# Performance work log

Hardware: AMD Instinct MI355X
Metric: run time of the kernel (lower is better)

## Reference

```python
import jax, jax.numpy as jnp
import numpy as np

N = 50000
E = 800000
D_IN = 1000
D_H2 = 128  # h_dim * multiple
D_H = 16


def gat_conv(x, src, dst, W, attn_l, attn_r, bias, n):
    """DGL-style GATConv (no dropout, no activation). Returns [n, H, F]."""
    H, F = attn_l.shape
    feat = (x @ W).reshape(n, H, F)                      # [N,H,F]
    el = jnp.sum(feat * attn_l[None], axis=-1)           # [N,H]
    er = jnp.sum(feat * attn_r[None], axis=-1)           # [N,H]
    e = jax.nn.leaky_relu(el[src] + er[dst], 0.2)        # [E,H]
    emax = jax.ops.segment_max(e, dst, num_segments=n)   # [N,H] per-dst softmax max
    ee = jnp.exp(e - emax[dst])                          # [E,H]
    denom = jax.ops.segment_sum(ee, dst, num_segments=n) # [N,H]
    alpha = ee / denom[dst]                              # [E,H]
    msg = feat[src] * alpha[..., None]                   # [E,H,F]
    out = jax.ops.segment_sum(msg, dst, num_segments=n)  # [N,H,F]
    return out + bias.reshape(1, H, F)


def setup_inputs() -> dict:
    key = jax.random.key(0)
    ks = jax.random.split(key, 24)
    rn = lambda k, shp, s=0.05: (jax.random.normal(k, shp, dtype=jnp.float32) * s)
    inp = {
        "x": rn(ks[0], (N, D_IN), 1.0),
        "src": jax.random.randint(ks[1], (E,), 0, N, dtype=jnp.int32),
        "dst": jax.random.randint(ks[2], (E,), 0, N, dtype=jnp.int32),
        "W1": rn(ks[3], (D_IN, D_H2)),
        "al1": rn(ks[4], (1, D_H2)),
        "ar1": rn(ks[5], (1, D_H2)),
        "b1": jnp.zeros((D_H2,), jnp.float32),
        "W2": rn(ks[6], (D_H2, 2 * D_H2)),
        "al2": rn(ks[7], (2, D_H2)),
        "ar2": rn(ks[8], (2, D_H2)),
        "b2": jnp.zeros((2 * D_H2,), jnp.float32),
        "Wm": rn(ks[9], (D_H2, 2 * D_H)),
        "alm": rn(ks[10], (2, D_H)),
        "arm": rn(ks[11], (2, D_H)),
        "bm": jnp.zeros((2 * D_H,), jnp.float32),
        "Wv": rn(ks[12], (D_H2, 2 * D_H)),
        "alv": rn(ks[13], (2, D_H)),
        "arv": rn(ks[14], (2, D_H)),
        "bv": jnp.zeros((2 * D_H,), jnp.float32),
        "eps": rn(ks[15], (N, D_H), 1.0),
    }
    return inp


def reference(x, src, dst, W1, al1, ar1, b1, W2, al2, ar2, b2,
              Wm, alm, arm, bm, Wv, alv, arv, bv, eps):
    n = x.shape[0]
    o = gat_conv(x, src, dst, W1, al1, ar1, b1, n).mean(-2)           # [N,128]
    o = gat_conv(o, src, dst, W2, al2, ar2, b2, n).mean(-2) + o       # residual
    mean = gat_conv(o, src, dst, Wm, alm, arm, bm, n).mean(-2)        # [N,16]
    var = jnp.exp(gat_conv(o, src, dst, Wv, alv, arv, bv, n).mean(-2))
    z = mean + jnp.sqrt(var) * eps                                    # reparameterize
    return z, mean, var
```

## Files before the change

### kernel.cpp

```cpp
#include <hip/hip_runtime.h>
#include <hip/hip_bf16.h>
#include <math.h>

typedef unsigned short u16;
typedef unsigned int u32;
typedef __attribute__((ext_vector_type(8))) __bf16 bf16x8;
typedef __attribute__((ext_vector_type(4))) float f32x4;
typedef __attribute__((ext_vector_type(4))) u32 u32x4;

#define NNODES 50000
#define NEDGES 800000

__device__ __forceinline__ float bf2f(u16 u) {
    union { u32 i; float f; } v; v.i = ((u32)u) << 16; return v.f;
}
__device__ __forceinline__ u16 f2bf(float x) {
    union { float f; u32 i; } v; v.f = x;
    u32 r = v.i + 0x7fffu + ((v.i >> 16) & 1u);
    return (u16)(r >> 16);
}
__device__ __forceinline__ float lrelu(float x) { return x >= 0.f ? x : 0.2f * x; }

__global__ __launch_bounds__(256) void k_zero(int* a, int count) {
    int i = blockIdx.x * 256 + threadIdx.x;
    if (i < count) a[i] = 0;
}

__global__ __launch_bounds__(256) void k_count(const int* __restrict__ dst, int* __restrict__ counts, int e) {
    int i = blockIdx.x * 256 + threadIdx.x;
    if (i < e) atomicAdd(&counts[dst[i]], 1);
}

__global__ __launch_bounds__(256) void k_scan1(const int* __restrict__ counts, int* __restrict__ row_ptr,
                                               int* __restrict__ bsums, int n) {
    __shared__ int tmp[256];
    int t = threadIdx.x, i = blockIdx.x * 256 + t;
    int v = (i < n) ? counts[i] : 0;
    tmp[t] = v; __syncthreads();
    for (int off = 1; off < 256; off <<= 1) {
        int x = 0; if (t >= off) x = tmp[t - off];
        __syncthreads(); tmp[t] += x; __syncthreads();
    }
    if (i < n) row_ptr[i] = tmp[t] - v;
    if (t == 255) bsums[blockIdx.x] = tmp[255];
}

__global__ __launch_bounds__(256) void k_scan2(int* bsums, int nb) {
    __shared__ int tmp[256];
    int t = threadIdx.x;
    int v = (t < nb) ? bsums[t] : 0;
    tmp[t] = v; __syncthreads();
    for (int off = 1; off < 256; off <<= 1) {
        int x = 0; if (t >= off) x = tmp[t - off];
        __syncthreads(); tmp[t] += x; __syncthreads();
    }
    if (t < nb) bsums[t] = tmp[t] - v;
}

__global__ __launch_bounds__(256) void k_scan3(int* __restrict__ row_ptr, const int* __restrict__ bsums,
                                               int n, int total) {
    int i = blockIdx.x * 256 + threadIdx.x;
    if (i < n) row_ptr[i] += bsums[blockIdx.x];
    if (i == 0) row_ptr[n] = total;
}

__global__ __launch_bounds__(256) void k_fill(const int* __restrict__ src, const int* __restrict__ dst,
                                              const int* __restrict__ row_ptr, int* __restrict__ cursor,
                                              int* __restrict__ esrc, int e) {
    int i = blockIdx.x * 256 + threadIdx.x;
    if (i < e) {
        int d = dst[i];
        int p = row_ptr[d] + atomicAdd(&cursor[d], 1);
        esrc[p] = src[i];
    }
}

__global__ __launch_bounds__(256) void k_transpose(const float* __restrict__ W, u16* __restrict__ Wt, int K, int Nn) {
    int i = blockIdx.x * 256 + threadIdx.x;
    if (i < K * Nn) { int k = i / Nn, n = i % Nn; Wt[n * K + k] = f2bf(W[i]); }
}

__global__ __launch_bounds__(256) void k_attnvec(const float* __restrict__ W2, const float* __restrict__ al2,
                                                 const float* __restrict__ ar2, const float* __restrict__ b2,
                                                 float* __restrict__ ul, float* __restrict__ ur,
                                                 float* __restrict__ bmean) {
    int t = threadIdx.x;
    int h = t >> 7, k = t & 127;
    const float* wrow = W2 + (size_t)k * 256 + h * 128;
    const float* alh = al2 + h * 128;
    const float* arh = ar2 + h * 128;
    float sl = 0.f, sr = 0.f;
    for (int f = 0; f < 128; f += 4) {
        f32x4 w = *(const f32x4*)(wrow + f);
        f32x4 a = *(const f32x4*)(alh + f);
        f32x4 r = *(const f32x4*)(arh + f);
#pragma unroll
        for (int q = 0; q < 4; q++) { sl += w[q] * a[q]; sr += w[q] * r[q]; }
    }
    ul[t] = sl; ur[t] = sr;
    if (t < 128) bmean[t] = 0.5f * (b2[t] + b2[128 + t]);
}

__global__ __launch_bounds__(256) void k_makeWc(const float* __restrict__ W2, u16* __restrict__ Wct) {
    int i = blockIdx.x * 256 + threadIdx.x;
    if (i < 128 * 256) {
        int f = i >> 8, c = i & 255, h = c >> 7, k = c & 127;
        Wct[i] = f2bf(0.5f * W2[(size_t)k * 256 + h * 128 + f]);
    }
}

__device__ __forceinline__ void load_af(const float* __restrict__ arow, int k0, int K, bf16x8& a) {
    if (k0 + 8 <= K) {
        f32x4 a0 = *(const f32x4*)(arow + k0);
        f32x4 a1 = *(const f32x4*)(arow + k0 + 4);
#pragma unroll
        for (int j = 0; j < 4; j++) { a[j] = (__bf16)a0[j]; a[4 + j] = (__bf16)a1[j]; }
    } else {
#pragma unroll
        for (int j = 0; j < 8; j++) a[j] = (__bf16)0.f;
    }
}
__device__ __forceinline__ void load_af(const u16* __restrict__ arow, int k0, int K, bf16x8& a) {
    if (k0 + 8 <= K) a = *(const bf16x8*)(arow + k0);
    else {
#pragma unroll
        for (int j = 0; j < 8; j++) a[j] = (__bf16)0.f;
    }
}

template <typename AT, bool EPI>
__global__ __launch_bounds__(256) void k_gemm_tiled(const AT* __restrict__ A, const u16* __restrict__ Bt,
                                                    u16* __restrict__ C, int M, int Nn, int K,
                                                    const float* __restrict__ bias,
                                                    const u16* __restrict__ resid) {
    __shared__ __align__(16) u16 lb[2][128 * 40];
    const int tid = threadIdx.x;
    const int wave = tid >> 6, lane = tid & 63;
    const int m = lane & 15, quad = lane >> 4;
    const int row0 = blockIdx.x * 64 + wave * 16;
    const int col0 = blockIdx.y * 128;

    f32x4 acc[8];
#pragma unroll
    for (int t = 0; t < 8; t++)
#pragma unroll
        for (int r = 0; r < 4; r++) acc[t][r] = 0.f;

    int ar = row0 + m; if (ar > M - 1) ar = M - 1;
    const AT* arow = A + (size_t)ar * K;
    const int scol = tid & 127;
    const int sseg = (tid >> 7) * 16;
    const u16* bcol = Bt + (size_t)(col0 + scol) * K;

    const int nsteps = (K + 31) >> 5;

#pragma unroll
    for (int p = 0; p < 2; ++p) {
        int kl = sseg + p * 8;
        u32x4 v = 0;
        if (kl < K) v = *(const u32x4*)(bcol + kl);
        *(u32x4*)&lb[0][scol * 40 + kl] = v;
    }
    bf16x8 acur, anext;
    load_af(arow, quad * 8, K, acur);
    __syncthreads();

    for (int s = 0; s < nsteps; ++s) {
        const int buf = s & 1;
        if (s + 1 < nsteps) {
            const int k0n = (s + 1) * 32;
            load_af(arow, k0n + quad * 8, K, anext);
#pragma unroll
            for (int p = 0; p < 2; ++p) {
                int kl = sseg + p * 8;
                u32x4 v = 0;
                if (k0n + kl < K) v = *(const u32x4*)(bcol + k0n + kl);
                *(u32x4*)&lb[buf ^ 1][scol * 40 + kl] = v;
            }
        }
#pragma unroll
        for (int t = 0; t < 8; ++t) {
            bf16x8 b = *(const bf16x8*)&lb[buf][(t * 16 + m) * 40 + quad * 8];
            acc[t] = __builtin_amdgcn_mfma_f32_16x16x32_bf16(acur, b, acc[t], 0, 0, 0);
        }
        acur = anext;
        __syncthreads();
    }

#pragma unroll
    for (int t = 0; t < 8; t++)
#pragma unroll
        for (int r = 0; r < 4; r++) {
            int row = row0 + quad * 4 + r;
            int col = col0 + t * 16 + m;
            if (row < M) {
                float v = acc[t][r];
                if (EPI) v += bias[col] + bf2f(resid[(size_t)row * Nn + col]);
                C[(size_t)row * Nn + col] = f2bf(v);
            }
        }
}

template <int NT>
__global__ __launch_bounds__(64) void k_gemm(const u16* __restrict__ A, const u16* __restrict__ Bt,
                                             u16* __restrict__ C, int M, int Nn, int K) {
    int row0 = blockIdx.x * 16;
    int col0 = blockIdx.y * (16 * NT);
    int lane = threadIdx.x;
    int m = lane & 15, quad = lane >> 4;
    f32x4 acc[NT];
#pragma unroll
    for (int t = 0; t < NT; t++)
#pragma unroll
        for (int r = 0; r < 4; r++) acc[t][r] = 0.f;

    const u16* arow = A + (size_t)(row0 + m) * K + quad * 8;
    int full = K >> 5;
    for (int s = 0; s < full; ++s) {
        bf16x8 a = *(const bf16x8*)(arow + s * 32);
#pragma unroll
        for (int t = 0; t < NT; t++) {
            bf16x8 b = *(const bf16x8*)(Bt + (size_t)(col0 + t * 16 + m) * K + s * 32 + quad * 8);
            acc[t] = __builtin_amdgcn_mfma_f32_16x16x32_bf16(a, b, acc[t], 0, 0, 0);
        }
    }
#pragma unroll
    for (int t = 0; t < NT; t++)
#pragma unroll
        for (int r = 0; r < 4; r++) {
            int row = row0 + quad * 4 + r;
            int col = col0 + t * 16 + m;
            if (row < M) C[(size_t)row * Nn + col] = f2bf(acc[t][r]);
        }
}

__global__ __launch_bounds__(256) void k_eler1(const u16* __restrict__ feat, const float* __restrict__ al,
                                               const float* __restrict__ ar, float* __restrict__ el,
                                               float* __restrict__ er, int n) {
    int node = blockIdx.x * 4 + (threadIdx.x >> 6);
    if (node >= n) return;
    int lane = threadIdx.x & 63;
    const u16* fr = feat + (size_t)node * 128;
    float f0 = bf2f(fr[lane]), f1 = bf2f(fr[64 + lane]);
    float pe = f0 * al[lane] + f1 * al[64 + lane];
    float pr = f0 * ar[lane] + f1 * ar[64 + lane];
#pragma unroll
    for (int off = 32; off; off >>= 1) { pe += __shfl_xor(pe, off); pr += __shfl_xor(pr, off); }
    if (lane == 0) { el[node] = pe; er[node] = pr; }
}

__global__ __launch_bounds__(256) void k_eler2o(const u16* __restrict__ o_in, const float* __restrict__ ul,
                                                const float* __restrict__ ur, float* __restrict__ el,
                                                float* __restrict__ er, int n) {
    int node = blockIdx.x * 4 + (threadIdx.x >> 6);
    if (node >= n) return;
    int lane = threadIdx.x & 63;
    const u16* fr = o_in + (size_t)node * 128;
    float f0 = bf2f(fr[lane]), f1 = bf2f(fr[64 + lane]);
#pragma unroll
    for (int h = 0; h < 2; ++h) {
        float pe = f0 * ul[h * 128 + lane] + f1 * ul[h * 128 + 64 + lane];
        float pr = f0 * ur[h * 128 + lane] + f1 * ur[h * 128 + 64 + lane];
#pragma unroll
        for (int off = 32; off; off >>= 1) { pe += __shfl_xor(pe, off); pr += __shfl_xor(pr, off); }
        if (lane == 0) { el[node * 2 + h] = pe; er[node * 2 + h] = pr; }
    }
}

__global__ __launch_bounds__(256) void k_elermv(const u16* __restrict__ featm, const u16* __restrict__ featv,
                                                const float* __restrict__ alm, const float* __restrict__ arm,
                                                const float* __restrict__ alv, const float* __restrict__ arv,
                                                float* __restrict__ elm, float* __restrict__ erm,
                                                float* __restrict__ elv, float* __restrict__ erv, int n) {
    int node = blockIdx.x * 4 + (threadIdx.x >> 6);
    if (node >= n) return;
    int lane = threadIdx.x & 63;
    int tbl = lane >> 5, j = lane & 31;
    const u16* ft = tbl ? featv : featm;
    const float* al = tbl ? alv : alm;
    const float* ar = tbl ? arv : arm;
    float f = bf2f(ft[(size_t)node * 32 + j]);
    float pe = f * al[j], pr = f * ar[j];
#pragma unroll
    for (int off = 1; off < 16; off <<= 1) { pe += __shfl_xor(pe, off); pr += __shfl_xor(pr, off); }
    if ((lane & 15) == 0) {
        int h = (lane >> 4) & 1;
        float* el = tbl ? elv : elm; float* er = tbl ? erv : erm;
        el[node * 2 + h] = pe; er[node * 2 + h] = pr;
    }
}

__global__ __launch_bounds__(256) void k_agg1(const int* __restrict__ row_ptr, const int* __restrict__ esrc,
                                              const u16* __restrict__ feat, const float* __restrict__ el,
                                              const float* __restrict__ er, const float* __restrict__ bias,
                                              u16* __restrict__ o_bf, int n) {
    int node = blockIdx.x * 4 + (threadIdx.x >> 6);
    if (node >= n) return;
    int lane = threadIdx.x & 63;
    int beg = row_ptr[node], end = row_ptr[node + 1];
    float erd = er[node];
    float mx = -3.0e38f;
    for (int i = beg + lane; i < end; i += 64) mx = fmaxf(mx, el[esrc[i]]);
#pragma unroll
    for (int off = 32; off; off >>= 1) mx = fmaxf(mx, __shfl_xor(mx, off));
    float me = (end > beg) ? lrelu(mx + erd) : 0.f;
    float acc0 = 0.f, acc1 = 0.f, den = 0.f;
    for (int base = beg; base < end; base += 64) {
        int i = base + lane;
        float w = 0.f; int s = 0;
        if (i < end) { s = esrc[i]; w = expf(lrelu(el[s] + erd) - me); }
        den += w;
        int cnt = min(64, end - base);
        int j = 0;
        for (; j + 4 <= cnt; j += 4) {
            float w0 = __shfl(w, j), w1 = __shfl(w, j + 1), w2 = __shfl(w, j + 2), w3 = __shfl(w, j + 3);
            int s0 = __shfl(s, j), s1 = __shfl(s, j + 1), s2 = __shfl(s, j + 2), s3 = __shfl(s, j + 3);
            u32 p0 = ((const u32*)(feat + (size_t)s0 * 128))[lane];
            u32 p1 = ((const u32*)(feat + (size_t)s1 * 128))[lane];
            u32 p2 = ((const u32*)(feat + (size_t)s2 * 128))[lane];
            u32 p3 = ((const u32*)(feat + (size_t)s3 * 128))[lane];
            acc0 += w0 * bf2f((u16)(p0 & 0xffff)) + w1 * bf2f((u16)(p1 & 0xffff))
                  + w2 * bf2f((u16)(p2 & 0xffff)) + w3 * bf2f((u16)(p3 & 0xffff));
            acc1 += w0 * bf2f((u16)(p0 >> 16)) + w1 * bf2f((u16)(p1 >> 16))
                  + w2 * bf2f((u16)(p2 >> 16)) + w3 * bf2f((u16)(p3 >> 16));
        }
        for (; j < cnt; ++j) {
            float wj = __shfl(w, j);
            int sj = __shfl(s, j);
            u32 pv = ((const u32*)(feat + (size_t)sj * 128))[lane];
            acc0 += wj * bf2f((u16)(pv & 0xffff));
            acc1 += wj * bf2f((u16)(pv >> 16));
        }
    }
#pragma unroll
    for (int off = 32; off; off >>= 1) den += __shfl_xor(den, off);
    float inv = (den > 0.f) ? 1.f / den : 0.f;
    float o0 = acc0 * inv + bias[2 * lane];
    float o1 = acc1 * inv + bias[2 * lane + 1];
    u32 pv = (u32)f2bf(o0) | ((u32)f2bf(o1) << 16);
    ((u32*)(o_bf + (size_t)node * 128))[lane] = pv;
}

__global__ __launch_bounds__(256) void k_agg2o(const int* __restrict__ row_ptr, const int* __restrict__ esrc,
                                               const u16* __restrict__ o_in, const float* __restrict__ el,
                                               const float* __restrict__ er, u16* __restrict__ agg, int n) {
    int node = blockIdx.x * 4 + (threadIdx.x >> 6);
    if (node >= n) return;
    int lane = threadIdx.x & 63;
    int beg = row_ptr[node], end = row_ptr[node + 1];
    float er0 = er[node * 2], er1 = er[node * 2 + 1];
    float mx0 = -3.0e38f, mx1 = -3.0e38f;
    for (int i = beg + lane; i < end; i += 64) {
        int s = esrc[i];
        float2 e2 = *(const float2*)(el + 2 * s);
        mx0 = fmaxf(mx0, e2.x); mx1 = fmaxf(mx1, e2.y);
    }
#pragma unroll
    for (int off = 32; off; off >>= 1) { mx0 = fmaxf(mx0, __shfl_xor(mx0, off)); mx1 = fmaxf(mx1, __shfl_xor(mx1, off)); }
    float me0 = (end > beg) ? lrelu(mx0 + er0) : 0.f;
    float me1 = (end > beg) ? lrelu(mx1 + er1) : 0.f;
    float a00 = 0.f, a01 = 0.f, a10 = 0.f, a11 = 0.f, d0 = 0.f, d1 = 0.f;
    for (int base = beg; base < end; base += 64) {
        int i = base + lane;
        float w0 = 0.f, w1 = 0.f; int s = 0;
        if (i < end) {
            s = esrc[i];
            float2 e2 = *(const float2*)(el + 2 * s);
            w0 = expf(lrelu(e2.x + er0) - me0);
            w1 = expf(lrelu(e2.y + er1) - me1);
        }
        d0 += w0; d1 += w1;
        int cnt = min(64, end - base);
        int j = 0;
        for (; j + 4 <= cnt; j += 4) {
            float w0a = __shfl(w0, j), w0b = __shfl(w0, j + 1), w0c = __shfl(w0, j + 2), w0d = __shfl(w0, j + 3);
            float w1a = __shfl(w1, j), w1b = __shfl(w1, j + 1), w1c = __shfl(w1, j + 2), w1d = __shfl(w1, j + 3);
            int sa = __shfl(s, j), sb = __shfl(s, j + 1), sc = __shfl(s, j + 2), sd = __shfl(s, j + 3);
            u32 pa = ((const u32*)(o_in + (size_t)sa * 128))[lane];
            u32 pb = ((const u32*)(o_in + (size_t)sb * 128))[lane];
            u32 pc = ((const u32*)(o_in + (size_t)sc * 128))[lane];
            u32 pd = ((const u32*)(o_in + (size_t)sd * 128))[lane];
            float la = bf2f((u16)(pa & 0xffff)), ha = bf2f((u16)(pa >> 16));
            float lb = bf2f((u16)(pb & 0xffff)), hb = bf2f((u16)(pb >> 16));
            float lc = bf2f((u16)(pc & 0xffff)), hc = bf2f((u16)(pc >> 16));
            float ld = bf2f((u16)(pd & 0xffff)), hd = bf2f((u16)(pd >> 16));
            a00 += w0a * la + w0b * lb + w0c * lc + w0d * ld;
            a01 += w0a * ha + w0b * hb + w0c * hc + w0d * hd;
            a10 += w1a * la + w1b * lb + w1c * lc + w1d * ld;
            a11 += w1a * ha + w1b * hb + w1c * hc + w1d * hd;
        }
        for (; j < cnt; ++j) {
            float w0j = __shfl(w0, j), w1j = __shfl(w1, j);
            int sj = __shfl(s, j);
            u32 pv = ((const u32*)(o_in + (size_t)sj * 128))[lane];
            float lo = bf2f((u16)(pv & 0xffff)), hi = bf2f((u16)(pv >> 16));
            a00 += w0j * lo; a01 += w0j * hi;
            a10 += w1j * lo; a11 += w1j * hi;
        }
    }
#pragma unroll
    for (int off = 32; off; off >>= 1) { d0 += __shfl_xor(d0, off); d1 += __shfl_xor(d1, off); }
    float i0 = (d0 > 0.f) ? 1.f / d0 : 0.f, i1 = (d1 > 0.f) ? 1.f / d1 : 0.f;
    u32 p0 = (u32)f2bf(a00 * i0) | ((u32)f2bf(a01 * i0) << 16);
    u32 p1 = (u32)f2bf(a10 * i1) | ((u32)f2bf(a11 * i1) << 16);
    u32* aw = (u32*)(agg + (size_t)node * 256);
    aw[lane] = p0;
    aw[64 + lane] = p1;
}

__global__ __launch_bounds__(256) void k_aggmv(const int* __restrict__ row_ptr, const int* __restrict__ esrc,
                                               const u16* __restrict__ featm, const u16* __restrict__ featv,
                                               const float* __restrict__ elm, const float* __restrict__ erm,
                                               const float* __restrict__ elv, const float* __restrict__ erv,
                                               const float* __restrict__ bm, const float* __restrict__ bv,
                                               const float* __restrict__ eps, float* __restrict__ out, int n) {
    int node = blockIdx.x * 4 + (threadIdx.x >> 6);
    if (node >= n) return;
    int lane = threadIdx.x & 63;
    int f = lane & 15, h = (lane >> 4) & 1, tbl = lane >> 5;
    int beg = row_ptr[node], end = row_ptr[node + 1];
    float erm0 = erm[2 * node], erm1 = erm[2 * node + 1];
    float erv0 = erv[2 * node], erv1 = erv[2 * node + 1];
    float mm0 = -3.0e38f, mm1 = -3.0e38f, mv0 = -3.0e38f, mv1 = -3.0e38f;
    for (int i = beg + lane; i < end; i += 64) {
        int s = esrc[i];
        float2 em = *(const float2*)(elm + 2 * s);
        float2 ev = *(const float2*)(elv + 2 * s);
        mm0 = fmaxf(mm0, em.x); mm1 = fmaxf(mm1, em.y);
        mv0 = fmaxf(mv0, ev.x); mv1 = fmaxf(mv1, ev.y);
    }
#pragma unroll
    for (int off = 32; off; off >>= 1) {
        mm0 = fmaxf(mm0, __shfl_xor(mm0, off)); mm1 = fmaxf(mm1, __shfl_xor(mm1, off));
        mv0 = fmaxf(mv0, __shfl_xor(mv0, off)); mv1 = fmaxf(mv1, __shfl_xor(mv1, off));
    }
    float mem0 = (end > beg) ? lrelu(mm0 + erm0) : 0.f;
    float mem1 = (end > beg) ? lrelu(mm1 + erm1) : 0.f;
    float mev0 = (end > beg) ? lrelu(mv0 + erv0) : 0.f;
    float mev1 = (end > beg) ? lrelu(mv1 + erv1) : 0.f;

    const u16* ftp = tbl ? featv : featm;
    const int fidx = h * 16 + f;
    float accv = 0.f;
    float dm0 = 0.f, dm1 = 0.f, dv0 = 0.f, dv1 = 0.f;
    for (int base = beg; base < end; base += 64) {
        int i = base + lane;
        float wm0 = 0.f, wm1 = 0.f, wv0 = 0.f, wv1 = 0.f; int s = 0;
        if (i < end) {
            s = esrc[i];
            float2 em = *(const float2*)(elm + 2 * s);
            float2 ev = *(const float2*)(elv + 2 * s);
            wm0 = expf(lrelu(em.x + erm0) - mem0);
            wm1 = expf(lrelu(em.y + erm1) - mem1);
            wv0 = expf(lrelu(ev.x + erv0) - mev0);
            wv1 = expf(lrelu(ev.y + erv1) - mev1);
        }
        dm0 += wm0; dm1 += wm1; dv0 += wv0; dv1 += wv1;
        int cnt = min(64, end - base);
        for (int j = 0; j < cnt; ++j) {
            int sj = __shfl(s, j);
            float bm0 = __shfl(wm0, j);
            float bm1 = __shfl(wm1, j);
            float bv0 = __shfl(wv0, j);
            float bv1 = __shfl(wv1, j);
            float wj = tbl ? (h ? bv1 : bv0) : (h ? bm1 : bm0);
            accv += wj * bf2f(ftp[(size_t)sj * 32 + fidx]);
        }
    }
#pragma unroll
    for (int off = 32; off; off >>= 1) {
        dm0 += __shfl_xor(dm0, off); dm1 += __shfl_xor(dm1, off);
        dv0 += __shfl_xor(dv0, off); dv1 += __shfl_xor(dv1, off);
    }
    float den = tbl ? (h ? dv1 : dv0) : (h ? dm1 : dm0);
    float inv = (den > 0.f) ? 1.f / den : 0.f;
    float biasc = tbl ? bv[fidx] : bm[fidx];
    float outc = accv * inv + biasc;
    float hm = 0.5f * (outc + __shfl_xor(outc, 16));
    float meanv = __shfl(hm, f);
    float varp = __shfl(hm, 32 + f);
    if (lane < 16) {
        float var = expf(varp);
        float z = meanv + sqrtf(var) * eps[(size_t)node * 16 + f];
        size_t base = (size_t)node * 16 + f;
        out[base] = z;
        out[(size_t)NNODES * 16 + base] = meanv;
        out[(size_t)2 * NNODES * 16 + base] = var;
    }
}

extern "C" void kernel_launch(void* const* d_in, const int* in_sizes, int n_in,
                              void* d_out, int out_size, void* d_ws, size_t ws_size,
                              hipStream_t stream) {
    const int N = NNODES, E = NEDGES;
    const float* x   = (const float*)d_in[0];
    const int* src   = (const int*)d_in[1];
    const int* dst   = (const int*)d_in[2];
    const float* W1  = (const float*)d_in[3];
    const float* al1 = (const float*)d_in[4];
    const float* ar1 = (const float*)d_in[5];
    const float* b1  = (const float*)d_in[6];
    const float* W2  = (const float*)d_in[7];
    const float* al2 = (const float*)d_in[8];
    const float* ar2 = (const float*)d_in[9];
    const float* b2  = (const float*)d_in[10];
    const float* Wm  = (const float*)d_in[11];
    const float* alm = (const float*)d_in[12];
    const float* arm = (const float*)d_in[13];
    const float* bm  = (const float*)d_in[14];
    const float* Wv  = (const float*)d_in[15];
    const float* alv = (const float*)d_in[16];
    const float* arv = (const float*)d_in[17];
    const float* bv  = (const float*)d_in[18];
    const float* eps = (const float*)d_in[19];
    float* out = (float*)d_out;

    char* ws = (char*)d_ws;
    size_t off = 0;
    auto take = [&](size_t bytes) { size_t r = off; off += (bytes + 255) & ~(size_t)255; return r; };
    int* counts   = (int*)(ws + take((size_t)N * 4));
    int* cursor   = (int*)(ws + take((size_t)N * 4));
    int* row_ptr  = (int*)(ws + take((size_t)(N + 1) * 4));
    int* bsums    = (int*)(ws + take(256 * 4));
    int* esrc     = (int*)(ws + take((size_t)E * 4));
    u16* W1t      = (u16*)(ws + take((size_t)128 * 1000 * 2));
    u16* Wct      = (u16*)(ws + take((size_t)128 * 256 * 2));
    u16* Wmt      = (u16*)(ws + take((size_t)32 * 128 * 2));
    u16* Wvt      = (u16*)(ws + take((size_t)32 * 128 * 2));
    float* ul2    = (float*)(ws + take(256 * 4));
    float* ur2    = (float*)(ws + take(256 * 4));
    float* bmean  = (float*)(ws + take(128 * 4));
    float* el1    = (float*)(ws + take((size_t)N * 4));
    float* er1    = (float*)(ws + take((size_t)N * 4));
    float* el2    = (float*)(ws + take((size_t)N * 2 * 4));
    float* er2    = (float*)(ws + take((size_t)N * 2 * 4));
    float* elm    = (float*)(ws + take((size_t)N * 2 * 4));
    float* erm    = (float*)(ws + take((size_t)N * 2 * 4));
    float* elv    = (float*)(ws + take((size_t)N * 2 * 4));
    float* erv    = (float*)(ws + take((size_t)N * 2 * 4));
    u16* o_bf     = (u16*)(ws + take((size_t)N * 128 * 2));
    u16* o2_bf    = (u16*)(ws + take((size_t)N * 128 * 2));
    u16* R        = (u16*)(ws + take((size_t)N * 256 * 2));
    u16* feat1    = R;
    u16* agg      = R;
    u16* featm    = R;
    u16* featv    = R + (size_t)N * 32;
    (void)ws_size; (void)n_in; (void)in_sizes; (void)out_size;

    const int nb = (N + 255) / 256;
    const int eb = (E + 255) / 256;
    const int wb = (N + 3) / 4;
    const int gb = (N + 63) / 64;

    k_zero<<<dim3(nb), 256, 0, stream>>>(counts, N);
    k_zero<<<dim3(nb), 256, 0, stream>>>(cursor, N);
    k_count<<<dim3(eb), 256, 0, stream>>>(dst, counts, E);
    k_scan1<<<dim3(nb), 256, 0, stream>>>(counts, row_ptr, bsums, N);
    k_scan2<<<dim3(1), 256, 0, stream>>>(bsums, nb);
    k_scan3<<<dim3(nb), 256, 0, stream>>>(row_ptr, bsums, N, E);
    k_fill<<<dim3(eb), 256, 0, stream>>>(src, dst, row_ptr, cursor, esrc, E);

    k_transpose<<<dim3((1000 * 128 + 255) / 256), 256, 0, stream>>>(W1, W1t, 1000, 128);
    k_makeWc<<<dim3(128), 256, 0, stream>>>(W2, Wct);
    k_attnvec<<<dim3(1), 256, 0, stream>>>(W2, al2, ar2, b2, ul2, ur2, bmean);
    k_transpose<<<dim3((128 * 32 + 255) / 256), 256, 0, stream>>>(Wm, Wmt, 128, 32);
    k_transpose<<<dim3((128 * 32 + 255) / 256), 256, 0, stream>>>(Wv, Wvt, 128, 32);

    k_gemm_tiled<float, false><<<dim3(gb, 1), 256, 0, stream>>>(x, W1t, feat1, N, 128, 1000, nullptr, nullptr);
    k_eler1<<<dim3(wb), 256, 0, stream>>>(feat1, al1, ar1, el1, er1, N);
    k_agg1<<<dim3(wb), 256, 0, stream>>>(row_ptr, esrc, feat1, el1, er1, b1, o_bf, N);

    k_eler2o<<<dim3(wb), 256, 0, stream>>>(o_bf, ul2, ur2, el2, er2, N);
    k_agg2o<<<dim3(wb), 256, 0, stream>>>(row_ptr, esrc, o_bf, el2, er2, agg, N);
    k_gemm_tiled<u16, true><<<dim3(gb, 1), 256, 0, stream>>>(agg, Wct, o2_bf, N, 128, 256, bmean, o_bf);

    k_gemm<2><<<dim3(N / 16, 1), 64, 0, stream>>>(o2_bf, Wmt, featm, N, 32, 128);
    k_gemm<2><<<dim3(N / 16, 1), 64, 0, stream>>>(o2_bf, Wvt, featv, N, 32, 128);
    k_elermv<<<dim3(wb), 256, 0, stream>>>(featm, featv, alm, arm, alv, arv, elm, erm, elv, erv, N);
    k_aggmv<<<dim3(wb), 256, 0, stream>>>(row_ptr, esrc, featm, featv, elm, erm, elv, erv,
                                          bm, bv, eps, out, N);
}
```

Measured before the change: 678.2 us.

## Fuse attention-score computation into GEMM and aggregation epilogues, merge prep kernels

Computes el/er for layer 1 inside the first GEMM epilogue, computes layer-2 el/er inside the layer-1 aggregation kernel, and merges the mean/var GEMMs with their attention scores into a single kernel. The weight transposes and attention-vector precomputation are merged into one prep kernel, and the two zeroing kernels become one. The aim is to remove several kernel launches and the extra passes that reread the feature matrices. In exchange the epilogues take extra shuffles and register pressure.

```diff
diff --git a/kernel.cpp b/kernel.cpp
--- a/kernel.cpp
+++ b/kernel.cpp
@@ -21,9 +21,9 @@
 }
 __device__ __forceinline__ float lrelu(float x) { return x >= 0.f ? x : 0.2f * x; }
 
-__global__ __launch_bounds__(256) void k_zero(int* a, int count) {
+__global__ __launch_bounds__(256) void k_zero2(int* a, int* b, int count) {
     int i = blockIdx.x * 256 + threadIdx.x;
-    if (i < count) a[i] = 0;
+    if (i < count) { a[i] = 0; b[i] = 0; }
 }
 
 __global__ __launch_bounds__(256) void k_count(const int* __restrict__ dst, int* __restrict__ counts, int e) {
@@ -75,37 +75,43 @@
     }
 }
 
-__global__ __launch_bounds__(256) void k_transpose(const float* __restrict__ W, u16* __restrict__ Wt, int K, int Nn) {
-    int i = blockIdx.x * 256 + threadIdx.x;
-    if (i < K * Nn) { int k = i / Nn, n = i % Nn; Wt[n * K + k] = f2bf(W[i]); }
-}
-
-__global__ __launch_bounds__(256) void k_attnvec(const float* __restrict__ W2, const float* __restrict__ al2,
-                                                 const float* __restrict__ ar2, const float* __restrict__ b2,
-                                                 float* __restrict__ ul, float* __restrict__ ur,
-                                                 float* __restrict__ bmean) {
-    int t = threadIdx.x;
-    int h = t >> 7, k = t & 127;
-    const float* wrow = W2 + (size_t)k * 256 + h * 128;
-    const float* alh = al2 + h * 128;
-    const float* arh = ar2 + h * 128;
-    float sl = 0.f, sr = 0.f;
-    for (int f = 0; f < 128; f += 4) {
-        f32x4 w = *(const f32x4*)(wrow + f);
-        f32x4 a = *(const f32x4*)(alh + f);
-        f32x4 r = *(const f32x4*)(arh + f);
-#pragma unroll
-        for (int q = 0; q < 4; q++) { sl += w[q] * a[q]; sr += w[q] * r[q]; }
-    }
-    ul[t] = sl; ur[t] = sr;
-    if (t < 128) bmean[t] = 0.5f * (b2[t] + b2[128 + t]);
-}
-
-__global__ __launch_bounds__(256) void k_makeWc(const float* __restrict__ W2, u16* __restrict__ Wct) {
-    int i = blockIdx.x * 256 + threadIdx.x;
-    if (i < 128 * 256) {
+__global__ __launch_bounds__(256) void k_prep(const float* __restrict__ W1, const float* __restrict__ W2,
+                                              const float* __restrict__ Wm, const float* __restrict__ Wv,
+                                              const float* __restrict__ al2, const float* __restrict__ ar2,
+                                              const float* __restrict__ b2,
+                                              u16* __restrict__ W1t, u16* __restrict__ Wct,
+                                              u16* __restrict__ Bmvt,
+                                              float* __restrict__ ul, float* __restrict__ ur,
+                                              float* __restrict__ bmean) {
+    int b = blockIdx.x, t = threadIdx.x;
+    if (b < 500) {
+        int i = b * 256 + t;
+        int k = i >> 7, n = i & 127;
+        W1t[(size_t)n * 1000 + k] = f2bf(W1[i]);
+    } else if (b < 628) {
+        int i = (b - 500) * 256 + t;
         int f = i >> 8, c = i & 255, h = c >> 7, k = c & 127;
         Wct[i] = f2bf(0.5f * W2[(size_t)k * 256 + h * 128 + f]);
+    } else if (b == 628) {
+        int h = t >> 7, k = t & 127;
+        const float* wrow = W2 + (size_t)k * 256 + h * 128;
+        const float* alh = al2 + h * 128;
+        const float* arh = ar2 + h * 128;
+        float sl = 0.f, sr = 0.f;
+        for (int f = 0; f < 128; f += 4) {
+            f32x4 w = *(const f32x4*)(wrow + f);
+            f32x4 a = *(const f32x4*)(alh + f);
+            f32x4 r = *(const f32x4*)(arh + f);
+#pragma unroll
+            for (int q = 0; q < 4; q++) { sl += w[q] * a[q]; sr += w[q] * r[q]; }
+        }
+        ul[t] = sl; ur[t] = sr;
+        if (t < 128) bmean[t] = 0.5f * (b2[t] + b2[128 + t]);
+    } else {
+        for (int i = t; i < 64 * 128; i += 256) {
+            int c = i >> 7, k = i & 127;
+            Bmvt[i] = f2bf(c < 32 ? Wm[(size_t)k * 32 + c] : Wv[(size_t)k * 32 + (c - 32)]);
+        }
     }
 }
 
@@ -128,11 +134,14 @@
     }
 }
 
-template <typename AT, bool EPI>
+template <typename AT, int MODE>
 __global__ __launch_bounds__(256) void k_gemm_tiled(const AT* __restrict__ A, const u16* __restrict__ Bt,
                                                     u16* __restrict__ C, int M, int Nn, int K,
                                                     const float* __restrict__ bias,
-                                                    const u16* __restrict__ resid) {
+                                                    const u16* __restrict__ resid,
+                                                    const float* __restrict__ al,
+                                                    const float* __restrict__ ar,
+                                                    float* __restrict__ el, float* __restrict__ er) {
     __shared__ __align__(16) u16 lb[2][128 * 40];
     const int tid = threadIdx.x;
     const int wave = tid >> 6, lane = tid & 63;
@@ -146,8 +155,8 @@
 #pragma unroll
         for (int r = 0; r < 4; r++) acc[t][r] = 0.f;
 
-    int ar = row0 + m; if (ar > M - 1) ar = M - 1;
-    const AT* arow = A + (size_t)ar * K;
+    int arr = row0 + m; if (arr > M - 1) arr = M - 1;
+    const AT* arow = A + (size_t)arr * K;
     const int scol = tid & 127;
     const int sseg = (tid >> 7) * 16;
     const u16* bcol = Bt + (size_t)(col0 + scol) * K;
@@ -188,112 +197,89 @@
     }
 
 #pragma unroll
-    for (int t = 0; t < 8; t++)
-#pragma unroll
-        for (int r = 0; r < 4; r++) {
-            int row = row0 + quad * 4 + r;
+    for (int r = 0; r < 4; r++) {
+        int row = row0 + quad * 4 + r;
+        if (MODE == 0) {
+            float pe = 0.f, pr = 0.f;
+#pragma unroll
+            for (int t = 0; t < 8; t++) {
+                float a = acc[t][r];
+                int c = col0 + t * 16 + m;
+                pe += a * al[c]; pr += a * ar[c];
+            }
+#pragma unroll
+            for (int off = 8; off; off >>= 1) { pe += __shfl_xor(pe, off); pr += __shfl_xor(pr, off); }
+            if (m == 0 && row < M) { el[row] = pe; er[row] = pr; }
+        }
+#pragma unroll
+        for (int t = 0; t < 8; t++) {
             int col = col0 + t * 16 + m;
             if (row < M) {
                 float v = acc[t][r];
-                if (EPI) v += bias[col] + bf2f(resid[(size_t)row * Nn + col]);
+                if (MODE == 1) v += bias[col] + bf2f(resid[(size_t)row * Nn + col]);
                 C[(size_t)row * Nn + col] = f2bf(v);
             }
         }
-}
-
-template <int NT>
-__global__ __launch_bounds__(64) void k_gemm(const u16* __restrict__ A, const u16* __restrict__ Bt,
-                                             u16* __restrict__ C, int M, int Nn, int K) {
+    }
+}
+
+__global__ __launch_bounds__(64) void k_gemmmv(const u16* __restrict__ A, const u16* __restrict__ Bt,
+                                               u16* __restrict__ featm, u16* __restrict__ featv,
+                                               const float* __restrict__ alm, const float* __restrict__ arm,
+                                               const float* __restrict__ alv, const float* __restrict__ arv,
+                                               float* __restrict__ elm, float* __restrict__ erm,
+                                               float* __restrict__ elv, float* __restrict__ erv, int M) {
     int row0 = blockIdx.x * 16;
-    int col0 = blockIdx.y * (16 * NT);
     int lane = threadIdx.x;
     int m = lane & 15, quad = lane >> 4;
-    f32x4 acc[NT];
-#pragma unroll
-    for (int t = 0; t < NT; t++)
+    f32x4 acc[4];
+#pragma unroll
+    for (int t = 0; t < 4; t++)
 #pragma unroll
         for (int r = 0; r < 4; r++) acc[t][r] = 0.f;
 
-    const u16* arow = A + (size_t)(row0 + m) * K + quad * 8;
-    int full = K >> 5;
-    for (int s = 0; s < full; ++s) {
+    const u16* arow = A + (size_t)(row0 + m) * 128 + quad * 8;
+#pragma unroll
+    for (int s = 0; s < 4; ++s) {
         bf16x8 a = *(const bf16x8*)(arow + s * 32);
 #pragma unroll
-        for (int t = 0; t < NT; t++) {
-            bf16x8 b = *(const bf16x8*)(Bt + (size_t)(col0 + t * 16 + m) * K + s * 32 + quad * 8);
+        for (int t = 0; t < 4; t++) {
+            bf16x8 b = *(const bf16x8*)(Bt + (size_t)(t * 16 + m) * 128 + s * 32 + quad * 8);
             acc[t] = __builtin_amdgcn_mfma_f32_16x16x32_bf16(a, b, acc[t], 0, 0, 0);
         }
     }
 #pragma unroll
-    for (int t = 0; t < NT; t++)
-#pragma unroll
-        for (int r = 0; r < 4; r++) {
-            int row = row0 + quad * 4 + r;
-            int col = col0 + t * 16 + m;
-            if (row < M) C[(size_t)row * Nn + col] = f2bf(acc[t][r]);
-        }
-}
-
-__global__ __launch_bounds__(256) void k_eler1(const u16* __restrict__ feat, const float* __restrict__ al,
-                                               const float* __restrict__ ar, float* __restrict__ el,
-                                               float* __restrict__ er, int n) {
-    int node = blockIdx.x * 4 + (threadIdx.x >> 6);
-    if (node >= n) return;
-    int lane = threadIdx.x & 63;
-    const u16* fr = feat + (size_t)node * 128;
-    float f0 = bf2f(fr[lane]), f1 = bf2f(fr[64 + lane]);
-    float pe = f0 * al[lane] + f1 * al[64 + lane];
-    float pr = f0 * ar[lane] + f1 * ar[64 + lane];
-#pragma unroll
-    for (int off = 32; off; off >>= 1) { pe += __shfl_xor(pe, off); pr += __shfl_xor(pr, off); }
-    if (lane == 0) { el[node] = pe; er[node] = pr; }
-}
-
-__global__ __launch_bounds__(256) void k_eler2o(const u16* __restrict__ o_in, const float* __restrict__ ul,
-                                                const float* __restrict__ ur, float* __restrict__ el,
-                                                float* __restrict__ er, int n) {
-    int node = blockIdx.x * 4 + (threadIdx.x >> 6);
-    if (node >= n) return;
-    int lane = threadIdx.x & 63;
-    const u16* fr = o_in + (size_t)node * 128;
-    float f0 = bf2f(fr[lane]), f1 = bf2f(fr[64 + lane]);
-#pragma unroll
-    for (int h = 0; h < 2; ++h) {
-        float pe = f0 * ul[h * 128 + lane] + f1 * ul[h * 128 + 64 + lane];
-        float pr = f0 * ur[h * 128 + lane] + f1 * ur[h * 128 + 64 + lane];
-#pragma unroll
-        for (int off = 32; off; off >>= 1) { pe += __shfl_xor(pe, off); pr += __shfl_xor(pr, off); }
-        if (lane == 0) { el[node * 2 + h] = pe; er[node * 2 + h] = pr; }
-    }
-}
-
-__global__ __launch_bounds__(256) void k_elermv(const u16* __restrict__ featm, const u16* __restrict__ featv,
-                                                const float* __restrict__ alm, const float* __restrict__ arm,
-                                                const float* __restrict__ alv, const float* __restrict__ arv,
-                                                float* __restrict__ elm, float* __restrict__ erm,
-                                                float* __restrict__ elv, float* __restrict__ erv, int n) {
-    int node = blockIdx.x * 4 + (threadIdx.x >> 6);
-    if (node >= n) return;
-    int lane = threadIdx.x & 63;
-    int tbl = lane >> 5, j = lane & 31;
-    const u16* ft = tbl ? featv : featm;
-    const float* al = tbl ? alv : alm;
-    const float* ar = tbl ? arv : arm;
-    float f = bf2f(ft[(size_t)node * 32 + j]);
-    float pe = f * al[j], pr = f * ar[j];
-#pragma unroll
-    for (int off = 1; off < 16; off <<= 1) { pe += __shfl_xor(pe, off); pr += __shfl_xor(pr, off); }
-    if ((lane & 15) == 0) {
-        int h = (lane >> 4) & 1;
-        float* el = tbl ? elv : elm; float* er = tbl ? erv : erm;
-        el[node * 2 + h] = pe; er[node * 2 + h] = pr;
+    for (int r = 0; r < 4; r++) {
+        int row = row0 + quad * 4 + r;
+#pragma unroll
+        for (int t = 0; t < 4; t++) {
+            float a = acc[t][r];
+            const float* alp = (t < 2) ? alm : alv;
+            const float* arp = (t < 2) ? arm : arv;
+            float pe = a * alp[(t & 1) * 16 + m];
+            float pr = a * arp[(t & 1) * 16 + m];
+#pragma unroll
+            for (int off = 8; off; off >>= 1) { pe += __shfl_xor(pe, off); pr += __shfl_xor(pr, off); }
+            if (m == 0 && row < M) {
+                float* elp = (t < 2) ? elm : elv;
+                float* erp = (t < 2) ? erm : erv;
+                elp[row * 2 + (t & 1)] = pe; erp[row * 2 + (t & 1)] = pr;
+            }
+            if (row < M) {
+                u16 v = f2bf(a);
+                if (t < 2) featm[(size_t)row * 32 + t * 16 + m] = v;
+                else       featv[(size_t)row * 32 + (t - 2) * 16 + m] = v;
+            }
+        }
     }
 }
 
 __global__ __launch_bounds__(256) void k_agg1(const int* __restrict__ row_ptr, const int* __restrict__ esrc,
                                               const u16* __restrict__ feat, const float* __restrict__ el,
                                               const float* __restrict__ er, const float* __restrict__ bias,
-                                              u16* __restrict__ o_bf, int n) {
+                                              const float* __restrict__ ul, const float* __restrict__ ur,
+                                              u16* __restrict__ o_bf, float* __restrict__ el2,
+                                              float* __restrict__ er2, int n) {
     int node = blockIdx.x * 4 + (threadIdx.x >> 6);
     if (node >= n) return;
     int lane = threadIdx.x & 63;
@@ -337,6 +323,14 @@
     float inv = (den > 0.f) ? 1.f / den : 0.f;
     float o0 = acc0 * inv + bias[2 * lane];
     float o1 = acc1 * inv + bias[2 * lane + 1];
+#pragma unroll
+    for (int h = 0; h < 2; ++h) {
+        float pe = o0 * ul[h * 128 + 2 * lane] + o1 * ul[h * 128 + 2 * lane + 1];
+        float pr = o0 * ur[h * 128 + 2 * lane] + o1 * ur[h * 128 + 2 * lane + 1];
+#pragma unroll
+        for (int off = 32; off; off >>= 1) { pe += __shfl_xor(pe, off); pr += __shfl_xor(pr, off); }
+        if (lane == 0) { el2[node * 2 + h] = pe; er2[node * 2 + h] = pr; }
+    }
     u32 pv = (u32)f2bf(o0) | ((u32)f2bf(o1) << 16);
     ((u32*)(o_bf + (size_t)node * 128))[lane] = pv;
 }
@@ -525,8 +519,7 @@
     int* esrc     = (int*)(ws + take((size_t)E * 4));
     u16* W1t      = (u16*)(ws + take((size_t)128 * 1000 * 2));
     u16* Wct      = (u16*)(ws + take((size_t)128 * 256 * 2));
-    u16* Wmt      = (u16*)(ws + take((size_t)32 * 128 * 2));
-    u16* Wvt      = (u16*)(ws + take((size_t)32 * 128 * 2));
+    u16* Bmvt     = (u16*)(ws + take((size_t)64 * 128 * 2));
     float* ul2    = (float*)(ws + take(256 * 4));
     float* ur2    = (float*)(ws + take(256 * 4));
     float* bmean  = (float*)(ws + take(128 * 4));
@@ -552,31 +545,26 @@
     const int wb = (N + 3) / 4;
     const int gb = (N + 63) / 64;
 
-    k_zero<<<dim3(nb), 256, 0, stream>>>(counts, N);
-    k_zero<<<dim3(nb), 256, 0, stream>>>(cursor, N);
+    k_prep<<<dim3(630), 256, 0, stream>>>(W1, W2, Wm, Wv, al2, ar2, b2, W1t, Wct, Bmvt, ul2, ur2, bmean);
+
+    k_zero2<<<dim3(nb), 256, 0, stream>>>(counts, cursor, N);
     k_count<<<dim3(eb), 256, 0, stream>>>(dst, counts, E);
     k_scan1<<<dim3(nb), 256, 0, stream>>>(counts, row_ptr, bsums, N);
     k_scan2<<<dim3(1), 256, 0, stream>>>(bsums, nb);
     k_scan3<<<dim3(nb), 256, 0, stream>>>(row_ptr, bsums, N, E);
     k_fill<<<dim3(eb), 256, 0, stream>>>(src, dst, row_ptr, cursor, esrc, E);
 
-    k_transpose<<<dim3((1000 * 128 + 255) / 256), 256, 0, stream>>>(W1, W1t, 1000, 128);
-    k_makeWc<<<dim3(128), 256, 0, stream>>>(W2, Wct);
-    k_attnvec<<<dim3(1), 256, 0, stream>>>(W2, al2, ar2, b2, ul2, ur2, bmean);
-    k_transpose<<<dim3((128 * 32 + 255) / 256), 256, 0, stream>>>(Wm, Wmt, 128, 32);
-    k_transpose<<<dim3((128 * 32 + 255) / 256), 256, 0, stream>>>(Wv, Wvt, 128, 32);
-
-    k_gemm_tiled<float, false><<<dim3(gb, 1), 256, 0, stream>>>(x, W1t, feat1, N, 128, 1000, nullptr, nullptr);
-    k_eler1<<<dim3(wb), 256, 0, stream>>>(feat1, al1, ar1, el1, er1, N);
-    k_agg1<<<dim3(wb), 256, 0, stream>>>(row_ptr, esrc, feat1, el1, er1, b1, o_bf, N);
-
-    k_eler2o<<<dim3(wb), 256, 0, stream>>>(o_bf, ul2, ur2, el2, er2, N);
+    k_gemm_tiled<float, 0><<<dim3(gb, 1), 256, 0, stream>>>(x, W1t, feat1, N, 128, 1000,
+                                                            nullptr, nullptr, al1, ar1, el1, er1);
+    k_agg1<<<dim3(wb), 256, 0, stream>>>(row_ptr, esrc, feat1, el1, er1, b1, ul2, ur2,
+                                         o_bf, el2, er2, N);
+
     k_agg2o<<<dim3(wb), 256, 0, stream>>>(row_ptr, esrc, o_bf, el2, er2, agg, N);
-    k_gemm_tiled<u16, true><<<dim3(gb, 1), 256, 0, stream>>>(agg, Wct, o2_bf, N, 128, 256, bmean, o_bf);
-
-    k_gemm<2><<<dim3(N / 16, 1), 64, 0, stream>>>(o2_bf, Wmt, featm, N, 32, 128);
-    k_gemm<2><<<dim3(N / 16, 1), 64, 0, stream>>>(o2_bf, Wvt, featv, N, 32, 128);
-    k_elermv<<<dim3(wb), 256, 0, stream>>>(featm, featv, alm, arm, alv, arv, elm, erm, elv, erv, N);
+    k_gemm_tiled<u16, 1><<<dim3(gb, 1), 256, 0, stream>>>(agg, Wct, o2_bf, N, 128, 256,
+                                                          bmean, o_bf, nullptr, nullptr, nullptr, nullptr);
+
+    k_gemmmv<<<dim3(N / 16), 64, 0, stream>>>(o2_bf, Bmvt, featm, featv, alm, arm, alv, arv,
+                                              elm, erm, elv, erv, N);
     k_aggmv<<<dim3(wb), 256, 0, stream>>>(row_ptr, esrc, featm, featv, elm, erm, elv, erv,
                                           bm, bv, eps, out, N);
 }
```

Result: faster. 650.7 us (-4.1%).
